# Performance work log

Measured on AMD Instinct MI355X. Metric: run time of the kernel, lower is better.

The kernel has to match this reference:

```python
import jax, jax.numpy as jnp
import numpy as np

B, C, H, W = 8, 256, 128, 128


def _bilinear_sample(img, gx, gy):
    """F.grid_sample(bilinear, padding_mode='zeros', align_corners=False).
    img: [B,C,H,W]; gx, gy: [B,H,W] normalized coords in [-1,1].
    Returns [B,C,H,W]."""
    Bi, Ci, Hi, Wi = img.shape
    ix = ((gx + 1.0) * Wi - 1.0) * 0.5  # pixel x coord
    iy = ((gy + 1.0) * Hi - 1.0) * 0.5  # pixel y coord
    ix0 = jnp.floor(ix)
    iy0 = jnp.floor(iy)
    wx1 = ix - ix0
    wy1 = iy - iy0
    bidx = jnp.arange(Bi)[:, None, None]

    def gather(iyf, ixf):
        valid = (ixf >= 0) & (ixf < Wi) & (iyf >= 0) & (iyf < Hi)
        iyc = jnp.clip(iyf, 0, Hi - 1).astype(jnp.int32)
        ixc = jnp.clip(ixf, 0, Wi - 1).astype(jnp.int32)
        v = img[bidx, :, iyc, ixc]  # [B,H,W,C]
        return jnp.where(valid[..., None], v, jnp.zeros((), img.dtype))

    v00 = gather(iy0, ix0)
    v01 = gather(iy0, ix0 + 1)
    v10 = gather(iy0 + 1, ix0)
    v11 = gather(iy0 + 1, ix0 + 1)
    w00 = ((1.0 - wy1) * (1.0 - wx1))[..., None]
    w01 = ((1.0 - wy1) * wx1)[..., None]
    w10 = (wy1 * (1.0 - wx1))[..., None]
    w11 = (wy1 * wx1)[..., None]
    out = v00 * w00 + v01 * w01 + v10 * w10 + v11 * w11  # [B,H,W,C]
    return out.transpose(0, 3, 1, 2)


def setup_inputs() -> dict:
    key = jax.random.key(0)
    ks = jax.random.split(key, 7)
    s = 1.0 / np.sqrt(C)
    return {
        "x": jax.random.normal(ks[0], (B, C, H, W), jnp.float32),
        "w_dw": jax.random.normal(ks[1], (C,), jnp.float32) * s,        # depthwise 1x1, no bias
        "w_off": jax.random.normal(ks[2], (2, C), jnp.float32) * s,     # offset 1x1 conv C->2
        "b_off": jax.random.normal(ks[3], (2,), jnp.float32) * 0.1,
        "w_pc": jax.random.normal(ks[4], (C, C), jnp.float32) * s,      # pointwise 1x1, no bias
        "w_W": jax.random.normal(ks[5], (C, C), jnp.float32) * s,       # residual-merge 1x1 conv
        "b_W": jax.random.normal(ks[6], (C,), jnp.float32) * 0.1,
    }


def reference(x, w_dw, w_off, b_off, w_pc, w_W, b_W):
    # offset = tanh(Conv1x1(x)) -> one shared (dx, dy) field (group == inplanes)
    offset = jnp.tanh(jnp.einsum('oc,bchw->bohw', w_off, x) + b_off[None, :, None, None])
    # depthwise 1x1 conv (bias=False) == per-channel scale
    dw = x * w_dw[None, :, None, None]
    # base normalized grid: X varies along W, Y along H (np.meshgrid convention)
    gx_base = jnp.linspace(-1.0, 1.0, W)[None, None, :]  # [1,1,W]
    gy_base = jnp.linspace(-1.0, 1.0, H)[None, :, None]  # [1,H,1]
    gx = jnp.clip(gx_base + offset[:, 0], -1.0, 1.0)  # [B,H,W]
    gy = jnp.clip(gy_base + offset[:, 1], -1.0, 1.0)
    sampled = _bilinear_sample(dw, gx, gy)             # [B,C,H,W]
    out = jnp.einsum('oc,bchw->bohw', w_pc, sampled)   # pointwise conv
    out = jnp.einsum('oc,bchw->bohw', w_W, out) + b_W[None, :, None, None]
    return out + x
```

## Files before the change

### kernel.cpp

```cpp
#include <hip/hip_runtime.h>
#include <hip/hip_bf16.h>

#define Bn 8
#define Cn 256
#define Hn 128
#define Wn 128
#define HWn (Hn * Wn)

typedef __attribute__((ext_vector_type(8))) short bfrag8;
typedef __attribute__((ext_vector_type(8))) unsigned short u16x8;
typedef __attribute__((ext_vector_type(4))) float f32x4;
typedef __attribute__((ext_vector_type(4))) unsigned int u32x4;

__device__ __forceinline__ float bf2f(unsigned short u) {
    unsigned int v = ((unsigned int)u) << 16;
    return __builtin_bit_cast(float, v);
}
__device__ __forceinline__ unsigned short f2bf(float f) {
    unsigned int u = __builtin_bit_cast(unsigned int, f);
    unsigned int lsb = (u >> 16) & 1u;
    u += 0x7fffu + lsb;
    return (unsigned short)(u >> 16);
}

__device__ __forceinline__ void load_lds16(const void* g, void* l) {
    __builtin_amdgcn_global_load_lds(
        (const __attribute__((address_space(1))) unsigned int*)g,
        (__attribute__((address_space(3))) unsigned int*)l,
        16, 0, 0);
}

__global__ __launch_bounds__(256)
void build_wcomb(const float* __restrict__ w_dw,
                 const float* __restrict__ w_pc,
                 const float* __restrict__ w_W,
                 unsigned short* __restrict__ wfrag) {
    const int o = blockIdx.x;
    const int c = threadIdx.x;
    float acc = 0.f;
#pragma unroll 8
    for (int k = 0; k < Cn; ++k)
        acc = fmaf(w_W[o * Cn + k], w_pc[k * Cn + c], acc);
    const int ob = o >> 4, lr = o & 15;
    const int ks = c >> 5, lg = (c & 31) >> 3, e = c & 7;
    const int lane = (lg << 4) + lr;
    wfrag[((((ob << 3) + ks) << 6) + lane) * 8 + e] = f2bf(acc * w_dw[c]);
}

__global__ __launch_bounds__(512, 1)
void prep_kernel(const float* __restrict__ x,
                 const float* __restrict__ w_off,
                 const float* __restrict__ b_off,
                 unsigned short* __restrict__ x_t,
                 float2* __restrict__ coords) {
    __shared__ __align__(16) char bufs[2][32 * 512 * 4];
    __shared__ float wo[2][256];
    const int t = threadIdx.x;
    const int lane = t & 63;
    const int wv = t >> 6;
    int blk = blockIdx.x;
    blk = ((blk & 7) << 5) | (blk >> 3);
    const int b = blk >> 5;
    const int p0 = (blk & 31) << 9;
    const float* xp = x + ((size_t)b * Cn) * HWn + p0;

    wo[t >> 8][t & 255] = w_off[t];

    float s0 = 0.f, s1 = 0.f;

    auto dma = [&](int sl, char* buf) {
#pragma unroll
        for (int i = 0; i < 4; ++i) {
            const int cl = (wv << 2) + i;
            const float* src = xp + (size_t)((sl << 5) + cl) * HWn + (lane << 2);
            load_lds16(src,       buf + (cl << 11));
            load_lds16(src + 256, buf + (cl << 11) + 1024);
        }
    };

    auto conv = [&](int sl, const char* buf) {
        const float* bf = (const float*)buf;
        u16x8 res[4];
#pragma unroll
        for (int s = 0; s < 32; ++s) {
            float v = bf[(s << 9) + t];
            s0 = fmaf(v, wo[0][(sl << 5) + s], s0);
            s1 = fmaf(v, wo[1][(sl << 5) + s], s1);
            res[s >> 3][s & 7] = f2bf(v);
        }
        unsigned short* dst = x_t + ((size_t)(b * HWn + p0 + t)) * Cn + (sl << 5);
#pragma unroll
        for (int j = 0; j < 4; ++j)
            *reinterpret_cast<u32x4*>(dst + (j << 3)) = __builtin_bit_cast(u32x4, res[j]);
    };

    dma(0, bufs[0]);
    __syncthreads();
#pragma unroll
    for (int sl = 1; sl < 8; ++sl) {
        dma(sl, bufs[sl & 1]);
        conv(sl - 1, bufs[(sl - 1) & 1]);
        __syncthreads();
    }
    conv(7, bufs[1]);

    float o0 = tanhf(s0 + b_off[0]);
    float o1 = tanhf(s1 + b_off[1]);
    int p = p0 + t;
    int yy = p >> 7, xx = p & 127;
    float gx = fminf(fmaxf(-1.f + xx * (2.f / 127.f) + o0, -1.f), 1.f);
    float gy = fminf(fmaxf(-1.f + yy * (2.f / 127.f) + o1, -1.f), 1.f);
    coords[(size_t)b * HWn + p] = make_float2(gx * 64.f + 63.5f, gy * 64.f + 63.5f);
}

__global__ __launch_bounds__(512, 2)
void main_kernel(const float* __restrict__ x,
                 const float* __restrict__ b_W,
                 const unsigned short* __restrict__ x_t,
                 const float2* __restrict__ coords,
                 const unsigned short* __restrict__ wfrag,
                 float* __restrict__ out) {
    __shared__ __align__(16) char As[4][32 * 512];
    __shared__ __align__(16) float4 wts[32];
    const int t = threadIdx.x;
    const int lane = t & 63;
    const int wid = t >> 6;
    int blk = blockIdx.x;
    blk = ((blk & 7) << 9) | (blk >> 3);
    const int b = blk >> 9;
    const int p0 = (blk & 511) << 5;
    const size_t pixbase = (size_t)b * HWn + p0;
    const unsigned short* xtb = x_t + (size_t)b * HWn * Cn;

    if (t < 32) {
        float2 co = coords[pixbase + t];
        float ix = co.x, iy = co.y;
        float fx = floorf(ix), fy = floorf(iy);
        int ix0 = (int)fx, iy0 = (int)fy;
        float wx1 = ix - fx, wy1 = iy - fy;
        float wx0 = 1.f - wx1, wy0 = 1.f - wy1;
        bool vx0 = (ix0 >= 0) && (ix0 < Wn);
        bool vx1 = (ix0 >= -1) && (ix0 < Wn - 1);
        bool vy0 = (iy0 >= 0) && (iy0 < Hn);
        bool vy1 = (iy0 >= -1) && (iy0 < Hn - 1);
        float4 w;
        w.x = (vy0 && vx0) ? wy0 * wx0 : 0.f;
        w.y = (vy0 && vx1) ? wy0 * wx1 : 0.f;
        w.z = (vy1 && vx0) ? wy1 * wx0 : 0.f;
        w.w = (vy1 && vx1) ? wy1 * wx1 : 0.f;
        wts[t] = w;
    }

    {
        const int hp = lane >> 5;
        const int j = lane & 31;
        float2 co[2];
#pragma unroll
        for (int i = 0; i < 2; ++i)
            co[i] = coords[pixbase + (wid << 2) + (i << 1) + hp];

#pragma unroll
        for (int i = 0; i < 2; ++i) {
            const int p = (wid << 2) + (i << 1);
            const int px = p + hp;
            float ix = co[i].x, iy = co[i].y;
            int ix0 = (int)floorf(ix), iy0 = (int)floorf(iy);
            int cx0 = min(max(ix0, 0), Wn - 1), cx1 = min(max(ix0 + 1, 0), Wn - 1);
            int cy0 = min(max(iy0, 0), Hn - 1), cy1 = min(max(iy0 + 1, 0), Hn - 1);
            const int gch = (j ^ (px & 15)) << 3;
            const unsigned short* s00 = xtb + (size_t)(cy0 * Wn + cx0) * Cn + gch;
            const unsigned short* s01 = xtb + (size_t)(cy0 * Wn + cx1) * Cn + gch;
            const unsigned short* s10 = xtb + (size_t)(cy1 * Wn + cx0) * Cn + gch;
            const unsigned short* s11 = xtb + (size_t)(cy1 * Wn + cx1) * Cn + gch;
            load_lds16(s00, &As[0][p << 9]);
            load_lds16(s01, &As[1][p << 9]);
            load_lds16(s10, &As[2][p << 9]);
            load_lds16(s11, &As[3][p << 9]);
        }
    }
    __syncthreads();

    {
        const int px = t >> 4;
        const float4 w = wts[px];
#pragma unroll
        for (int q = 0; q < 2; ++q) {
            const int kc = (t & 15) + (q << 4);
            const int off = (px << 9) + ((kc ^ (px & 15)) << 4);
            u16x8 c00 = *reinterpret_cast<const u16x8*>(&As[0][off]);
            u16x8 c01 = *reinterpret_cast<const u16x8*>(&As[1][off]);
            u16x8 c10 = *reinterpret_cast<const u16x8*>(&As[2][off]);
            u16x8 c11 = *reinterpret_cast<const u16x8*>(&As[3][off]);
            u16x8 res;
#pragma unroll
            for (int e = 0; e < 8; ++e) {
                float r = w.x * bf2f(c00[e]) + w.y * bf2f(c01[e])
                        + w.z * bf2f(c10[e]) + w.w * bf2f(c11[e]);
                res[e] = f2bf(r);
            }
            *reinterpret_cast<u16x8*>(&As[0][off]) = res;
        }
    }
    __syncthreads();

    const int lr = lane & 15;
    const int lg = lane >> 4;
    f32x4 acc[2][2];
#pragma unroll
    for (int m = 0; m < 2; ++m)
#pragma unroll
        for (int n = 0; n < 2; ++n)
            acc[m][n] = (f32x4){0.f, 0.f, 0.f, 0.f};

#pragma unroll
    for (int ks = 0; ks < 8; ++ks) {
        bfrag8 a[2], bb[2];
        const int kc = (ks << 2) + lg;
#pragma unroll
        for (int n = 0; n < 2; ++n) {
            const int pr = (n << 4) + lr;
            const int off = (pr << 9) + ((kc ^ (pr & 15)) << 4);
            bb[n] = *reinterpret_cast<const bfrag8*>(&As[0][off]);
        }
#pragma unroll
        for (int m = 0; m < 2; ++m) {
            const int ob = (wid << 1) + m;
            const unsigned short* src = wfrag + ((((ob << 3) + ks) << 6) + lane) * 8;
            a[m] = *reinterpret_cast<const bfrag8*>(src);
        }
#pragma unroll
        for (int m = 0; m < 2; ++m)
#pragma unroll
            for (int n = 0; n < 2; ++n)
                acc[m][n] = __builtin_amdgcn_mfma_f32_16x16x32_bf16(a[m], bb[n], acc[m][n], 0, 0, 0);
    }

#pragma unroll
    for (int m = 0; m < 2; ++m) {
#pragma unroll
        for (int r = 0; r < 4; ++r) {
            int o = (wid << 5) + (m << 4) + (lg << 2) + r;
            float bw = b_W[o];
            size_t rowbase = ((size_t)b * Cn + o) * HWn + p0;
#pragma unroll
            for (int n = 0; n < 2; ++n) {
                size_t idx = rowbase + (n << 4) + lr;
                __builtin_nontemporal_store(acc[m][n][r] + bw + x[idx], &out[idx]);
            }
        }
    }
}

extern "C" void kernel_launch(void* const* d_in, const int* in_sizes, int n_in,
                              void* d_out, int out_size, void* d_ws, size_t ws_size,
                              hipStream_t stream) {
    const float* x     = (const float*)d_in[0];
    const float* w_dw  = (const float*)d_in[1];
    const float* w_off = (const float*)d_in[2];
    const float* b_off = (const float*)d_in[3];
    const float* w_pc  = (const float*)d_in[4];
    const float* w_W   = (const float*)d_in[5];
    const float* b_W   = (const float*)d_in[6];
    float* out = (float*)d_out;

    char* ws = (char*)d_ws;
    unsigned short* x_t   = (unsigned short*)ws;
    float2* coords        = (float2*)(ws + 67108864);
    unsigned short* wcomb = (unsigned short*)(ws + 67108864 + 1048576);

    build_wcomb<<<dim3(256), dim3(256), 0, stream>>>(w_dw, w_pc, w_W, wcomb);
    prep_kernel<<<dim3(256), dim3(512), 0, stream>>>(x, w_off, b_off, x_t, coords);
    main_kernel<<<dim3(4096), dim3(512), 0, stream>>>(x, b_W, x_t, coords, wcomb, out);
}
```

Baseline: 118.2 us.

## Retile prep kernel into smaller blocks with split-channel reduction and explicit waitcnt pipelining

The prep kernel now runs 1024 blocks of 256 threads, each covering 128 pixels instead of 512. The two halves of the block each handle 16 channels per 32-channel slice, and the offset-conv partial sums are combined through LDS. Double buffering now uses explicit vmcnt waits and raw barriers instead of __syncthreads. The aim is more blocks and waves per CU to hide global load latency in this memory-bound transpose/convert pass, at the cost of a small extra reduction step and shorter contiguous loads per row.

```diff
diff --git a/kernel.cpp b/kernel.cpp
--- a/kernel.cpp
+++ b/kernel.cpp
@@ -47,70 +47,88 @@
     wfrag[((((ob << 3) + ks) << 6) + lane) * 8 + e] = f2bf(acc * w_dw[c]);
 }
 
-__global__ __launch_bounds__(512, 1)
+__global__ __launch_bounds__(256, 4)
 void prep_kernel(const float* __restrict__ x,
                  const float* __restrict__ w_off,
                  const float* __restrict__ b_off,
                  unsigned short* __restrict__ x_t,
                  float2* __restrict__ coords) {
-    __shared__ __align__(16) char bufs[2][32 * 512 * 4];
+    __shared__ __align__(16) float tile[2][32 * 128];
     __shared__ float wo[2][256];
+    __shared__ float red[2][2][128];
     const int t = threadIdx.x;
     const int lane = t & 63;
     const int wv = t >> 6;
     int blk = blockIdx.x;
-    blk = ((blk & 7) << 5) | (blk >> 3);
-    const int b = blk >> 5;
-    const int p0 = (blk & 31) << 9;
+    blk = ((blk & 7) << 7) | (blk >> 3);
+    const int b = blk >> 7;
+    const int p0 = (blk & 127) << 7;
     const float* xp = x + ((size_t)b * Cn) * HWn + p0;
 
-    wo[t >> 8][t & 255] = w_off[t];
-
+    wo[0][t] = w_off[t];
+    wo[1][t] = w_off[256 + t];
+
+    const int px = t & 127;
+    const int h = t >> 7;
     float s0 = 0.f, s1 = 0.f;
 
-    auto dma = [&](int sl, char* buf) {
+    auto dma = [&](int p) {
+        float* buf = tile[p & 1];
+        const int r = lane >> 5;
+        const int q = lane & 31;
 #pragma unroll
         for (int i = 0; i < 4; ++i) {
-            const int cl = (wv << 2) + i;
-            const float* src = xp + (size_t)((sl << 5) + cl) * HWn + (lane << 2);
-            load_lds16(src,       buf + (cl << 11));
-            load_lds16(src + 256, buf + (cl << 11) + 1024);
+            const int cb = (wv << 3) + (i << 1);
+            const float* src = xp + (size_t)((p << 5) + cb + r) * HWn + (q << 2);
+            load_lds16(src, buf + (cb << 7));
         }
     };
 
-    auto conv = [&](int sl, const char* buf) {
-        const float* bf = (const float*)buf;
-        u16x8 res[4];
-#pragma unroll
-        for (int s = 0; s < 32; ++s) {
-            float v = bf[(s << 9) + t];
-            s0 = fmaf(v, wo[0][(sl << 5) + s], s0);
-            s1 = fmaf(v, wo[1][(sl << 5) + s], s1);
-            res[s >> 3][s & 7] = f2bf(v);
-        }
-        unsigned short* dst = x_t + ((size_t)(b * HWn + p0 + t)) * Cn + (sl << 5);
-#pragma unroll
-        for (int j = 0; j < 4; ++j)
-            *reinterpret_cast<u32x4*>(dst + (j << 3)) = __builtin_bit_cast(u32x4, res[j]);
+    auto conv = [&](int p) {
+        const float* buf = tile[p & 1];
+        u16x8 r0, r1;
+#pragma unroll
+        for (int j = 0; j < 16; ++j) {
+            const int cl = (h << 4) + j;
+            float v = buf[(cl << 7) + px];
+            s0 = fmaf(v, wo[0][(p << 5) + cl], s0);
+            s1 = fmaf(v, wo[1][(p << 5) + cl], s1);
+            if (j < 8) r0[j] = f2bf(v); else r1[j - 8] = f2bf(v);
+        }
+        unsigned short* dst = x_t + ((size_t)(b * HWn + p0 + px)) * Cn + (p << 5) + (h << 4);
+        *reinterpret_cast<u16x8*>(dst) = r0;
+        *reinterpret_cast<u16x8*>(dst + 8) = r1;
     };
 
-    dma(0, bufs[0]);
+    dma(0);
+#pragma unroll
+    for (int p = 0; p < 8; ++p) {
+        if (p < 7) {
+            dma(p + 1);
+            asm volatile("s_waitcnt vmcnt(4) lgkmcnt(0)" ::: "memory");
+        } else {
+            asm volatile("s_waitcnt vmcnt(0) lgkmcnt(0)" ::: "memory");
+        }
+        __builtin_amdgcn_sched_barrier(0);
+        __builtin_amdgcn_s_barrier();
+        __builtin_amdgcn_sched_barrier(0);
+        conv(p);
+        __builtin_amdgcn_s_barrier();
+        __builtin_amdgcn_sched_barrier(0);
+    }
+
+    red[h][0][px] = s0;
+    red[h][1][px] = s1;
     __syncthreads();
-#pragma unroll
-    for (int sl = 1; sl < 8; ++sl) {
-        dma(sl, bufs[sl & 1]);
-        conv(sl - 1, bufs[(sl - 1) & 1]);
-        __syncthreads();
-    }
-    conv(7, bufs[1]);
-
-    float o0 = tanhf(s0 + b_off[0]);
-    float o1 = tanhf(s1 + b_off[1]);
-    int p = p0 + t;
-    int yy = p >> 7, xx = p & 127;
-    float gx = fminf(fmaxf(-1.f + xx * (2.f / 127.f) + o0, -1.f), 1.f);
-    float gy = fminf(fmaxf(-1.f + yy * (2.f / 127.f) + o1, -1.f), 1.f);
-    coords[(size_t)b * HWn + p] = make_float2(gx * 64.f + 63.5f, gy * 64.f + 63.5f);
+    if (t < 128) {
+        float o0 = tanhf(red[0][0][t] + red[1][0][t] + b_off[0]);
+        float o1 = tanhf(red[0][1][t] + red[1][1][t] + b_off[1]);
+        int p = p0 + t;
+        int yy = p >> 7, xx = p & 127;
+        float gx = fminf(fmaxf(-1.f + xx * (2.f / 127.f) + o0, -1.f), 1.f);
+        float gy = fminf(fmaxf(-1.f + yy * (2.f / 127.f) + o1, -1.f), 1.f);
+        coords[(size_t)b * HWn + p] = make_float2(gx * 64.f + 63.5f, gy * 64.f + 63.5f);
+    }
 }
 
 __global__ __launch_bounds__(512, 2)
@@ -269,6 +287,6 @@
     unsigned short* wcomb = (unsigned short*)(ws + 67108864 + 1048576);
 
     build_wcomb<<<dim3(256), dim3(256), 0, stream>>>(w_dw, w_pc, w_W, wcomb);
-    prep_kernel<<<dim3(256), dim3(512), 0, stream>>>(x, w_off, b_off, x_t, coords);
+    prep_kernel<<<dim3(1024), dim3(256), 0, stream>>>(x, w_off, b_off, x_t, coords);
     main_kernel<<<dim3(4096), dim3(512), 0, stream>>>(x, b_W, x_t, coords, wcomb, out);
 }
```

Result: faster. 112.2 us (-5.1%).
